# Kernel tuning notes

Measured on AMD Instinct MI355X. Metric: run time of the kernel, lower is better.

The kernel has to match this reference:

```python
import jax, jax.numpy as jnp
import numpy as np

D_MODEL = 1024
NUM_HEADS = 16
D_K = D_MODEL // NUM_HEADS
THETA = 10000.0
BATCH, SEQ = 2, 2048


def apply_rope(x, token_positions, theta):
    # x: [..., heads, seq, d_k]; interleaved pair rotation
    d = x.shape[-1]
    inv_freq = theta ** (-jnp.arange(0, d, 2, dtype=jnp.float32) / d)  # [d/2]
    ang = token_positions.astype(jnp.float32)[:, None] * inv_freq[None, :]  # [seq, d/2]
    cos, sin = jnp.cos(ang), jnp.sin(ang)  # broadcast over batch/heads
    x_even = x[..., 0::2]
    x_odd = x[..., 1::2]
    out_even = x_even * cos - x_odd * sin
    out_odd = x_even * sin + x_odd * cos
    out = jnp.stack([out_even, out_odd], axis=-1)  # [..., seq, d/2, 2]
    return out.reshape(x.shape)


def setup_inputs() -> dict:
    key = jax.random.key(0)
    ks = jax.random.split(key, 5)
    scale = 1.0 / np.sqrt(D_MODEL)
    return {
        "x": jax.random.normal(ks[0], (BATCH, SEQ, D_MODEL), dtype=jnp.float32),
        "wq": jax.random.normal(ks[1], (D_MODEL, D_MODEL), dtype=jnp.float32) * scale,
        "wk": jax.random.normal(ks[2], (D_MODEL, D_MODEL), dtype=jnp.float32) * scale,
        "wv": jax.random.normal(ks[3], (D_MODEL, D_MODEL), dtype=jnp.float32) * scale,
        "wo": jax.random.normal(ks[4], (D_MODEL, D_MODEL), dtype=jnp.float32) * scale,
        "token_positions": jnp.arange(SEQ, dtype=jnp.int32),
    }


def reference(x, wq, wk, wv, wo, token_positions):
    B, S, _ = x.shape
    # fused-style QKV projections: weight layout is [d_out, d_in]
    xq = jnp.einsum("bsd,kd->bsk", x, wq)
    xk = jnp.einsum("bsd,kd->bsk", x, wk)
    xv = jnp.einsum("bsd,vd->bsv", x, wv)
    # split heads: [b, h, s, d_h]
    def split(t):
        return t.reshape(B, S, NUM_HEADS, D_K).transpose(0, 2, 1, 3)
    xq, xk, xv = split(xq), split(xk), split(xv)
    xq = apply_rope(xq, token_positions, THETA)
    xk = apply_rope(xk, token_positions, THETA)
    scores = jnp.einsum("bhqd,bhkd->bhqk", xq, xk) / jnp.sqrt(jnp.float32(D_K))
    causal = jnp.tril(jnp.ones((S, S), dtype=bool))
    scores = jnp.where(causal, scores, -jnp.inf)
    attn = jax.nn.softmax(scores, axis=-1)
    out = jnp.einsum("bhqk,bhkd->bhqd", attn, xv)
    out = out.transpose(0, 2, 1, 3).reshape(B, S, D_MODEL)  # merge heads
    return jnp.einsum("bsv,dv->bsd", out, wo)
```

## Files before the change

kernel.cpp:

```cpp
#include <hip/hip_runtime.h>

typedef __attribute__((ext_vector_type(8))) short short8;
typedef __attribute__((ext_vector_type(4))) short short4v;
typedef __attribute__((ext_vector_type(4))) float floatx4;

__device__ inline ushort f2b(float f) {
    union { uint i; float f; } c; c.f = f;
    uint i = c.i;
    uint r = (i + 0x7FFFu + ((i >> 16) & 1u)) >> 16;
    return (ushort)r;
}

__device__ __forceinline__ void load_lds16(const ushort* g, ushort* l) {
    __builtin_amdgcn_global_load_lds((const __attribute__((address_space(1))) void*)g,
                                     (__attribute__((address_space(3))) void*)l, 16, 0, 0);
}

__global__ __launch_bounds__(256) void cvt4_k(const float* __restrict__ x,
                                              const float* __restrict__ wq,
                                              const float* __restrict__ wk,
                                              const float* __restrict__ wv,
                                              ushort* __restrict__ xb,
                                              ushort* __restrict__ wqb,
                                              ushort* __restrict__ wkb,
                                              ushort* __restrict__ wvb,
                                              const int* __restrict__ pos,
                                              float2* __restrict__ tab) {
    const int blk = blockIdx.x;
    if (blk >= 3584) {
        const int idx = (blk - 3584) * 256 + threadIdx.x;
        const int s = idx >> 5, fi = idx & 31;
        const float inv = exp2f(-(float)fi * 0.41524101186092557f);
        const float ang = (float)pos[s] * inv;
        float sn, cs;
        sincosf(ang, &sn, &cs);
        tab[idx] = make_float2(cs, sn);
        return;
    }
    const float* in; ushort* out; int base;
    if (blk < 2048)      { in = x;  out = xb;  base = blk; }
    else if (blk < 2560) { in = wq; out = wqb; base = blk - 2048; }
    else if (blk < 3072) { in = wk; out = wkb; base = blk - 2560; }
    else                 { in = wv; out = wvb; base = blk - 3072; }
    const int i = (base * 256 + threadIdx.x) * 8;
    float4 f0 = *(const float4*)(in + i);
    float4 f1 = *(const float4*)(in + i + 4);
    ushort u[8] = {f2b(f0.x), f2b(f0.y), f2b(f0.z), f2b(f0.w),
                   f2b(f1.x), f2b(f1.y), f2b(f1.z), f2b(f1.w)};
    *(uint4*)(out + i) = *(const uint4*)u;
}

__global__ __launch_bounds__(256) void cvt_k(const float* __restrict__ in,
                                             ushort* __restrict__ out, int n) {
    const int i = (blockIdx.x * 256 + threadIdx.x) * 8;
    if (i >= n) return;
    float4 f0 = *(const float4*)(in + i);
    float4 f1 = *(const float4*)(in + i + 4);
    ushort u[8] = {f2b(f0.x), f2b(f0.y), f2b(f0.z), f2b(f0.w),
                   f2b(f1.x), f2b(f1.y), f2b(f1.z), f2b(f1.w)};
    *(uint4*)(out + i) = *(const uint4*)u;
}

template <bool OUTF32>
__device__ __forceinline__ void gemm_body(ushort* As, ushort* Bs,
                                          const ushort* __restrict__ A,
                                          const ushort* __restrict__ B,
                                          void* __restrict__ C,
                                          int N, int m0, int n0,
                                          bool doRope, const float2* __restrict__ tab,
                                          float oscale) {
    const int tid = threadIdx.x;
    const int wave = tid >> 6, lane = tid & 63;
    const int quad = lane >> 4, l16 = lane & 15;
    const int wm = (wave >> 1) * 64, wn = (wave & 1) * 64;

    floatx4 acc[4][4] = {};

    const int cA = tid, cB = tid + 256;
    const int rA = cA >> 2, jgA = ((cA & 3) - (rA >> 1)) & 3;
    const int rB = cB >> 2, jgB = ((cB & 3) - (rB >> 1)) & 3;
    const ushort* gaA = A + (size_t)(m0 + rA) * 1024 + jgA * 8;
    const ushort* gaB = A + (size_t)(m0 + rB) * 1024 + jgB * 8;
    const ushort* gbA = B + (size_t)(n0 + rA) * 1024 + jgA * 8;
    const ushort* gbB = B + (size_t)(n0 + rB) * 1024 + jgB * 8;

    load_lds16(gaA, As + cA * 8);
    load_lds16(gaB, As + cB * 8);
    load_lds16(gbA, Bs + cA * 8);
    load_lds16(gbB, Bs + cB * 8);
    __syncthreads();

    for (int kt = 0; kt < 32; ++kt) {
        const int cur = kt & 1;
        if (kt + 1 < 32) {
            const int nb = (cur ^ 1) * 4096;
            load_lds16(gaA + (kt + 1) * 32, As + nb + cA * 8);
            load_lds16(gaB + (kt + 1) * 32, As + nb + cB * 8);
            load_lds16(gbA + (kt + 1) * 32, Bs + nb + cA * 8);
            load_lds16(gbB + (kt + 1) * 32, Bs + nb + cB * 8);
        }
        const ushort* as = As + cur * 4096;
        const ushort* bs = Bs + cur * 4096;
        short8 af[4], bf[4];
#pragma unroll
        for (int i = 0; i < 4; ++i) {
            const int ra = wm + i * 16 + l16;
            const int rb = wn + i * 16 + l16;
            af[i] = *(const short8*)(as + ra * 32 + (((quad + (ra >> 1)) & 3) << 3));
            bf[i] = *(const short8*)(bs + rb * 32 + (((quad + (rb >> 1)) & 3) << 3));
        }
#pragma unroll
        for (int mi = 0; mi < 4; ++mi)
#pragma unroll
            for (int ni = 0; ni < 4; ++ni)
                acc[mi][ni] = __builtin_amdgcn_mfma_f32_16x16x32_bf16(af[mi], bf[ni], acc[mi][ni], 0, 0, 0);
        __syncthreads();
    }
#pragma unroll
    for (int mi = 0; mi < 4; ++mi) {
        const int row = m0 + wm + mi * 16 + quad * 4;
#pragma unroll
        for (int ni = 0; ni < 4; ++ni) {
            const int col = n0 + wn + ni * 16 + l16;
            const int fi = ((wn + ni * 16 + l16) & 63) >> 1;
#pragma unroll
            for (int r = 0; r < 4; ++r) {
                float v = acc[mi][ni][r];
                if (doRope) {
                    const float other = __shfl_xor(v, 1);
                    const float2 cs = tab[((row + r) & 2047) * 32 + fi];
                    v = (col & 1) ? (other * cs.y + v * cs.x) : (v * cs.x - other * cs.y);
                }
                v *= oscale;
                if (OUTF32) ((float*)C)[(size_t)(row + r) * N + col] = v;
                else        ((ushort*)C)[(size_t)(row + r) * N + col] = f2b(v);
            }
        }
    }
}

__global__ __launch_bounds__(256) void gemm_qkv(const ushort* __restrict__ xb,
                                                const ushort* __restrict__ wqb,
                                                const ushort* __restrict__ wkb,
                                                const ushort* __restrict__ wvb,
                                                ushort* __restrict__ q,
                                                ushort* __restrict__ k,
                                                ushort* __restrict__ vt,
                                                const float2* __restrict__ tab) {
    __shared__ __align__(16) ushort As[8192], Bs[8192];
    const int blk = blockIdx.x;
    const int job = blk >> 8, r = blk & 255;
    const ushort *A, *B;
    ushort* C;
    int N, m0, n0;
    bool rope;
    float osc;
    if (job == 0)      { A = xb;  B = wqb; C = q;  N = 1024; m0 = (r >> 3) * 128; n0 = (r & 7) * 128; rope = true;  osc = 0.18033688011112042f; }
    else if (job == 1) { A = xb;  B = wkb; C = k;  N = 1024; m0 = (r >> 3) * 128; n0 = (r & 7) * 128; rope = true;  osc = 1.0f; }
    else               { A = wvb; B = xb;  C = vt; N = 4096; m0 = (r & 7) * 128;  n0 = (r >> 3) * 128; rope = false; osc = 1.0f; }
    gemm_body<false>(As, Bs, A, B, C, N, m0, n0, rope, tab, osc);
}

__global__ __launch_bounds__(256) void gemm_o(const ushort* __restrict__ A,
                                              const ushort* __restrict__ B,
                                              float* __restrict__ C) {
    __shared__ __align__(16) ushort As[8192], Bs[8192];
    gemm_body<true>(As, Bs, A, B, C, 1024, blockIdx.y * 128, blockIdx.x * 128, false, nullptr, 1.0f);
}

__global__ __launch_bounds__(256, 4) void attn_k(const ushort* __restrict__ Qg,
                                                 const ushort* __restrict__ Kg,
                                                 const ushort* __restrict__ Vtg,
                                                 ushort* __restrict__ Og) {
    __shared__ __align__(16) ushort Ks[2][4096];
    __shared__ __align__(16) ushort Vs[2][4096];

    const int tid = threadIdx.x;
    const int wave = tid >> 6, lane = tid & 63;
    const int quad = lane >> 4, l16 = lane & 15;
    const int blk = blockIdx.x;
    const int bh = blk & 31;
    const int qt = 31 - (blk >> 5);
    const int b = bh >> 4, h = bh & 15;
    const int bq = b * 2048;
    const int wl = wave * 16 + l16;
    const int nk = qt + 1, dt = nk - 1;

    const int cA = tid, cB = tid + 256;
    const int sA = cA >> 3, jA = ((cA & 7) - sA) & 7;
    const int sB = cB >> 3, jB = ((cB & 7) - sB) & 7;
    const ushort* kgA = Kg + (size_t)(bq + sA) * 1024 + h * 64 + jA * 8;
    const ushort* kgB = Kg + (size_t)(bq + sB) * 1024 + h * 64 + jB * 8;
    const ushort* vgA = Vtg + (size_t)(h * 64 + sA) * 4096 + bq + jA * 8;
    const ushort* vgB = Vtg + (size_t)(h * 64 + sB) * 4096 + bq + jB * 8;

    const int kb0 = l16 * 64 + (((quad + l16) & 7) << 3);
    const int kb1 = l16 * 64 + (((quad + 4 + l16) & 7) << 3);
    int vbs[4];
#pragma unroll
    for (int cb = 0; cb < 4; ++cb)
        vbs[cb] = l16 * 64 + (((cb * 2 + (quad >> 1) + l16) & 7) << 3) + (quad & 1) * 4;

    const ushort* qrow = Qg + (size_t)(bq + qt * 64 + wl) * 1024 + h * 64 + quad * 8;
    const short8 qf0 = *(const short8*)qrow;
    const short8 qf1 = *(const short8*)(qrow + 32);

    floatx4 od[4] = {};
    float l_st = 0.0f;

    load_lds16(kgA, &Ks[0][cA * 8]);
    load_lds16(kgB, &Ks[0][cB * 8]);
    load_lds16(vgA, &Vs[0][cA * 8]);
    load_lds16(vgB, &Vs[0][cB * 8]);
    __syncthreads();

    const ushort* kgA2 = kgA + 65536;
    const ushort* kgB2 = kgB + 65536;
    const ushort* vgA2 = vgA + 64;
    const ushort* vgB2 = vgB + 64;

    for (int kt = 0; kt < nk; ++kt) {
        const int cur = kt & 1;
        if (kt + 1 < nk) {
            const int nxt = cur ^ 1;
            load_lds16(kgA2, &Ks[nxt][cA * 8]);
            load_lds16(kgB2, &Ks[nxt][cB * 8]);
            load_lds16(vgA2, &Vs[nxt][cA * 8]);
            load_lds16(vgB2, &Vs[nxt][cB * 8]);
            kgA2 += 65536; kgB2 += 65536; vgA2 += 64; vgB2 += 64;
        }
        const ushort* kc = &Ks[cur][0];
        const ushort* vc = &Vs[cur][0];

        floatx4 st[4];
        __builtin_amdgcn_s_setprio(1);
#pragma unroll
        for (int cb = 0; cb < 4; ++cb) {
            short8 kf0 = *(const short8*)(kc + kb0 + cb * 1024);
            short8 kf1 = *(const short8*)(kc + kb1 + cb * 1024);
            floatx4 z = {};
            z = __builtin_amdgcn_mfma_f32_16x16x32_bf16(kf0, qf0, z, 0, 0, 0);
            z = __builtin_amdgcn_mfma_f32_16x16x32_bf16(kf1, qf1, z, 0, 0, 0);
            st[cb] = z;
        }
        __builtin_amdgcn_s_setprio(0);

        const bool diag = (kt == dt);
        float pv[4][4];
        float sum = 0.0f;
#pragma unroll
        for (int cb = 0; cb < 4; ++cb) {
            const int scb = cb * 16 + quad * 4;
#pragma unroll
            for (int r = 0; r < 4; ++r) {
                float e = exp2f(st[cb][r]);
                if (diag && (scb + r > wl)) e = 0.0f;
                pv[cb][r] = e;
                sum += e;
            }
        }
        sum += __shfl_xor(sum, 16);
        sum += __shfl_xor(sum, 32);
        l_st += sum;

        short4v pb[4];
#pragma unroll
        for (int cb = 0; cb < 4; ++cb) {
            uint lo_, hi_;
            asm("v_cvt_pk_bf16_f32 %0, %1, %2" : "=v"(lo_) : "v"(pv[cb][0]), "v"(pv[cb][1]));
            asm("v_cvt_pk_bf16_f32 %0, %1, %2" : "=v"(hi_) : "v"(pv[cb][2]), "v"(pv[cb][3]));
            union { uint u[2]; short4v s; } cvu;
            cvu.u[0] = lo_; cvu.u[1] = hi_;
            pb[cb] = cvu.s;
        }

        __builtin_amdgcn_s_setprio(1);
#pragma unroll
        for (int db = 0; db < 4; ++db) {
#pragma unroll
            for (int cb = 0; cb < 4; ++cb) {
                short4v vf = *(const short4v*)(vc + vbs[cb] + db * 1024);
                od[db] = __builtin_amdgcn_mfma_f32_16x16x16bf16_1k(vf, pb[cb], od[db], 0, 0, 0);
            }
        }
        __builtin_amdgcn_s_setprio(0);
        __syncthreads();
    }

    const float linv = 1.0f / l_st;
    ushort* orow = Og + (size_t)(bq + qt * 64 + wl) * 1024 + h * 64 + quad * 4;
#pragma unroll
    for (int db = 0; db < 4; ++db) {
        uint2 w;
        w.x = (uint)f2b(od[db][0] * linv) | ((uint)f2b(od[db][1] * linv) << 16);
        w.y = (uint)f2b(od[db][2] * linv) | ((uint)f2b(od[db][3] * linv) << 16);
        *(uint2*)(orow + db * 16) = w;
    }
}

extern "C" void kernel_launch(void* const* d_in, const int* in_sizes, int n_in,
                              void* d_out, int out_size, void* d_ws, size_t ws_size,
                              hipStream_t stream) {
    const float* x  = (const float*)d_in[0];
    const float* wq = (const float*)d_in[1];
    const float* wk = (const float*)d_in[2];
    const float* wv = (const float*)d_in[3];
    const float* wo = (const float*)d_in[4];
    const int* pos  = (const int*)d_in[5];

    const size_t NX = (size_t)4096 * 1024;
    const size_t NW = (size_t)1024 * 1024;

    ushort* q_ws  = (ushort*)d_ws;
    ushort* k_ws  = q_ws + NX;
    ushort* vt_ws = k_ws + NX;
    ushort* o_ws  = vt_ws + NX;
    ushort* xb  = (ushort*)d_out;
    ushort* wqb = xb + NX;
    ushort* wkb = wqb + NW;
    ushort* wvb = wkb + NW;
    float2* tab = (float2*)(wvb + NW);

    cvt4_k<<<dim3(3840), 256, 0, stream>>>(x, wq, wk, wv, xb, wqb, wkb, wvb, pos, tab);
    gemm_qkv<<<dim3(768), 256, 0, stream>>>(xb, wqb, wkb, wvb, q_ws, k_ws, vt_ws, tab);
    attn_k<<<dim3(1024), 256, 0, stream>>>(q_ws, k_ws, vt_ws, o_ws);
    cvt_k<<<dim3(512), 256, 0, stream>>>(wo, q_ws, (int)NW);
    gemm_o<<<dim3(8, 32), 256, 0, stream>>>(o_ws, q_ws, (float*)d_out);
}
```

Before: 201.2 us.

## Retile output GEMM to 128x64 blocks and peel diagonal attention step

The output projection GEMM gets its own kernel with 128x64 tiles and 512 blocks instead of 256 blocks of 128x128, so more blocks cover the GPU's compute units. It loads through global_load_lds into swizzled LDS with double buffering. The attention loop is split so the diagonal tile is handled in a separate final step, which removes the per-iteration diagonal check and the final barrier. The smaller tiles mean less data reuse per block, and the fp32 output stores are scalar.

```diff
diff --git a/kernel.cpp b/kernel.cpp
--- a/kernel.cpp
+++ b/kernel.cpp
@@ -164,8 +164,72 @@
 __global__ __launch_bounds__(256) void gemm_o(const ushort* __restrict__ A,
                                               const ushort* __restrict__ B,
                                               float* __restrict__ C) {
-    __shared__ __align__(16) ushort As[8192], Bs[8192];
-    gemm_body<true>(As, Bs, A, B, C, 1024, blockIdx.y * 128, blockIdx.x * 128, false, nullptr, 1.0f);
+    __shared__ __align__(16) ushort As[8192];
+    __shared__ __align__(16) ushort Bs[4096];
+
+    const int blk = blockIdx.x;
+    const int m0 = (blk >> 4) * 128, n0 = (blk & 15) * 64;
+
+    const int tid = threadIdx.x;
+    const int wave = tid >> 6, lane = tid & 63;
+    const int quad = lane >> 4, l16 = lane & 15;
+    const int wm = (wave >> 1) * 64, wn = (wave & 1) * 32;
+
+    floatx4 acc[4][2] = {};
+
+    const int cA1 = tid, cA2 = tid + 256, cBc = tid;
+    const int rA1 = cA1 >> 2, jg1 = ((cA1 & 3) - (rA1 >> 1)) & 3;
+    const int rA2 = cA2 >> 2, jg2 = ((cA2 & 3) - (rA2 >> 1)) & 3;
+    const int rBc = cBc >> 2, jgB = ((cBc & 3) - (rBc >> 1)) & 3;
+    const ushort* ga1 = A + (size_t)(m0 + rA1) * 1024 + jg1 * 8;
+    const ushort* ga2 = A + (size_t)(m0 + rA2) * 1024 + jg2 * 8;
+    const ushort* gb1 = B + (size_t)(n0 + rBc) * 1024 + jgB * 8;
+
+    load_lds16(ga1, As + cA1 * 8);
+    load_lds16(ga2, As + cA2 * 8);
+    load_lds16(gb1, Bs + cBc * 8);
+    __syncthreads();
+
+    for (int kt = 0; kt < 32; ++kt) {
+        const int cur = kt & 1;
+        if (kt + 1 < 32) {
+            const int nbA = (cur ^ 1) * 4096;
+            const int nbB = (cur ^ 1) * 2048;
+            load_lds16(ga1 + (kt + 1) * 32, As + nbA + cA1 * 8);
+            load_lds16(ga2 + (kt + 1) * 32, As + nbA + cA2 * 8);
+            load_lds16(gb1 + (kt + 1) * 32, Bs + nbB + cBc * 8);
+        }
+        const ushort* as = As + cur * 4096;
+        const ushort* bs = Bs + cur * 2048;
+        short8 af[4], bf[2];
+#pragma unroll
+        for (int i = 0; i < 4; ++i) {
+            const int ra = wm + i * 16 + l16;
+            af[i] = *(const short8*)(as + ra * 32 + (((quad + (ra >> 1)) & 3) << 3));
+        }
+#pragma unroll
+        for (int j = 0; j < 2; ++j) {
+            const int rb = wn + j * 16 + l16;
+            bf[j] = *(const short8*)(bs + rb * 32 + (((quad + (rb >> 1)) & 3) << 3));
+        }
+#pragma unroll
+        for (int mi = 0; mi < 4; ++mi)
+#pragma unroll
+            for (int ni = 0; ni < 2; ++ni)
+                acc[mi][ni] = __builtin_amdgcn_mfma_f32_16x16x32_bf16(af[mi], bf[ni], acc[mi][ni], 0, 0, 0);
+        __syncthreads();
+    }
+#pragma unroll
+    for (int mi = 0; mi < 4; ++mi) {
+        const int row = m0 + wm + mi * 16 + quad * 4;
+#pragma unroll
+        for (int ni = 0; ni < 2; ++ni) {
+            const int col = n0 + wn + ni * 16 + l16;
+#pragma unroll
+            for (int r = 0; r < 4; ++r)
+                C[(size_t)(row + r) * 1024 + col] = acc[mi][ni][r];
+        }
+    }
 }
 
 __global__ __launch_bounds__(256, 4) void attn_k(const ushort* __restrict__ Qg,
@@ -219,9 +283,9 @@
     const ushort* vgA2 = vgA + 64;
     const ushort* vgB2 = vgB + 64;
 
-    for (int kt = 0; kt < nk; ++kt) {
+    auto step = [&](int kt, bool diag, bool pref) {
         const int cur = kt & 1;
-        if (kt + 1 < nk) {
+        if (pref) {
             const int nxt = cur ^ 1;
             load_lds16(kgA2, &Ks[nxt][cA * 8]);
             load_lds16(kgB2, &Ks[nxt][cB * 8]);
@@ -245,7 +309,6 @@
         }
         __builtin_amdgcn_s_setprio(0);
 
-        const bool diag = (kt == dt);
         float pv[4][4];
         float sum = 0.0f;
 #pragma unroll
@@ -284,8 +347,11 @@
             }
         }
         __builtin_amdgcn_s_setprio(0);
-        __syncthreads();
-    }
+        if (pref) __syncthreads();
+    };
+
+    for (int kt = 0; kt < dt; ++kt) step(kt, false, true);
+    step(dt, true, false);
 
     const float linv = 1.0f / l_st;
     ushort* orow = Og + (size_t)(bq + qt * 64 + wl) * 1024 + h * 64 + quad * 4;
@@ -325,5 +391,5 @@
     gemm_qkv<<<dim3(768), 256, 0, stream>>>(xb, wqb, wkb, wvb, q_ws, k_ws, vt_ws, tab);
     attn_k<<<dim3(1024), 256, 0, stream>>>(q_ws, k_ws, vt_ws, o_ws);
     cvt_k<<<dim3(512), 256, 0, stream>>>(wo, q_ws, (int)NW);
-    gemm_o<<<dim3(8, 32), 256, 0, stream>>>(o_ws, q_ws, (float*)d_out);
-}
+    gemm_o<<<dim3(512), 256, 0, stream>>>(o_ws, q_ws, (float*)d_out);
+}
```

Result: faster. 197.1 us (-2.1%).
